# Performance work log

Measured on AMD Instinct MI355X. Metric: run time of the kernel, lower is better.

Reference implementation:

```python
import jax, jax.numpy as jnp
import numpy as np

KERNEL = 3  # 2*half_size + 1 with half_size=1
ITER = 20


def _pool(v):
    # MaxPool2d(kernel=3, stride=1, padding=1) == SAME max reduce_window on NCHW
    return jax.lax.reduce_window(v, -jnp.inf, jax.lax.max,
                                 (1, 1, KERNEL, KERNEL), (1, 1, 1, 1), 'SAME')


def _erode(v):
    return -_pool(-v)


def setup_inputs() -> dict:
    key = jax.random.key(0)
    x = jax.random.normal(key, (16, 1, 1024, 1024), dtype=jnp.float32)
    return {"x": x}


def reference(x):
    skel0 = x - _pool(_erode(x))  # open(x) = dilate(erode(x))

    def step(carry, _):
        xc, skel = carry
        xc = _erode(xc)
        skel = skel + (xc - _pool(_erode(xc)))
        return (xc, skel), None

    (_, skel), _ = jax.lax.scan(step, (x, skel0), None, length=ITER)
    return skel
```

## Files before the change

kernel.cpp:

```cpp
#include <hip/hip_runtime.h>


static constexpr int W = 1024, H = 1024, NIMG = 16;
static constexpr int RCH = 32;
static constexpr int NSTEP = RCH + 16;
static constexpr int WPB = 4;
static constexpr float BIG = 3.0e38f;

__device__ __forceinline__ float min3f(float a, float b, float c) { return fminf(fminf(a, b), c); }
__device__ __forceinline__ float max3f(float a, float b, float c) { return fmaxf(fmaxf(a, b), c); }

__device__ __forceinline__ float dpp_left(float v) {
    return __int_as_float(__builtin_amdgcn_mov_dpp(__float_as_int(v), 0x138, 0xF, 0xF, true));
}
__device__ __forceinline__ float dpp_right(float v) {
    return __int_as_float(__builtin_amdgcn_mov_dpp(__float_as_int(v), 0x130, 0xF, 0xF, true));
}

template<bool FIRST, bool WRITE_E, bool EDGE, bool LE, bool RE>
__device__ __forceinline__
void pipe_step2(int t, int y0, int gx,
                bool leftEdge, bool rightEdge, bool lane_ok,
                const float* __restrict__ in, float* __restrict__ eo,
                float* __restrict__ sk,
                float4 (&OB)[7], float4 (&MB)[7], float4& OD, float4& MD,
                float4 (&acc)[8], float4 (&pf)[2])
{
    float4 cur0, cur1;
    if (!EDGE || (unsigned)t < (unsigned)H)       cur0 = pf[0];
    else                                          cur0 = make_float4(BIG, BIG, BIG, BIG);
    if (!EDGE || (unsigned)(t + 1) < (unsigned)H) cur1 = pf[1];
    else                                          cur1 = make_float4(BIG, BIG, BIG, BIG);
    {
        const int n0 = t + 2, n1 = t + 3;
        if ((!EDGE || (unsigned)n0 < (unsigned)H) && n0 <= y0 + RCH + 7)
            pf[0] = *(const float4*)&in[(size_t)n0 * W + gx];
        if ((!EDGE || (unsigned)n1 < (unsigned)H) && n1 <= y0 + RCH + 7)
            pf[1] = *(const float4*)&in[(size_t)n1 * W + gx];
    }

#pragma unroll
    for (int s = 0; s < 7; ++s) {
        const float4 fOld = OB[s];
        const float4 fMid = MB[s];

        float4 vm0, vm1;
        vm0.x = min3f(fOld.x, fMid.x, cur0.x);
        vm0.y = min3f(fOld.y, fMid.y, cur0.y);
        vm0.z = min3f(fOld.z, fMid.z, cur0.z);
        vm0.w = min3f(fOld.w, fMid.w, cur0.w);
        vm1.x = min3f(fMid.x, cur0.x, cur1.x);
        vm1.y = min3f(fMid.y, cur0.y, cur1.y);
        vm1.z = min3f(fMid.z, cur0.z, cur1.z);
        vm1.w = min3f(fMid.w, cur0.w, cur1.w);
        float l0 = dpp_left(vm0.w), r0 = dpp_right(vm0.x);
        float l1 = dpp_left(vm1.w), r1 = dpp_right(vm1.x);
        if (LE && leftEdge)  { l0 = BIG; l1 = BIG; }
        if (RE && rightEdge) { r0 = BIG; r1 = BIG; }
        float4 en0, en1;
        en0.x = min3f(l0,    vm0.x, vm0.y);
        en0.y = min3f(vm0.x, vm0.y, vm0.z);
        en0.z = min3f(vm0.y, vm0.z, vm0.w);
        en0.w = min3f(vm0.z, vm0.w, r0);
        en1.x = min3f(l1,    vm1.x, vm1.y);
        en1.y = min3f(vm1.x, vm1.y, vm1.z);
        en1.z = min3f(vm1.y, vm1.z, vm1.w);
        en1.w = min3f(vm1.z, vm1.w, r1);

        float4 gOld, gMid;
        if (s < 6) { gOld = OB[s + 1]; gMid = MB[s + 1]; }
        else       { gOld = OD;        gMid = MD;        }
        float4 vx0, vx1;
        if (!EDGE) {
            vx0.x = max3f(gOld.x, gMid.x, en0.x);
            vx0.y = max3f(gOld.y, gMid.y, en0.y);
            vx0.z = max3f(gOld.z, gMid.z, en0.z);
            vx0.w = max3f(gOld.w, gMid.w, en0.w);
            vx1.x = max3f(gMid.x, en0.x, en1.x);
            vx1.y = max3f(gMid.y, en0.y, en1.y);
            vx1.z = max3f(gMid.z, en0.z, en1.z);
            vx1.w = max3f(gMid.w, en0.w, en1.w);
        } else {
            const bool topOK0 = (t - s - 3) >= 0, botOK0 = (t - s - 1) < H;
            const bool topOK1 = (t - s - 2) >= 0, botOK1 = (t - s) < H;
            vx0.x = max3f(topOK0 ? gOld.x : -BIG, gMid.x, botOK0 ? en0.x : -BIG);
            vx0.y = max3f(topOK0 ? gOld.y : -BIG, gMid.y, botOK0 ? en0.y : -BIG);
            vx0.z = max3f(topOK0 ? gOld.z : -BIG, gMid.z, botOK0 ? en0.z : -BIG);
            vx0.w = max3f(topOK0 ? gOld.w : -BIG, gMid.w, botOK0 ? en0.w : -BIG);
            vx1.x = max3f(topOK1 ? gMid.x : -BIG, en0.x, botOK1 ? en1.x : -BIG);
            vx1.y = max3f(topOK1 ? gMid.y : -BIG, en0.y, botOK1 ? en1.y : -BIG);
            vx1.z = max3f(topOK1 ? gMid.z : -BIG, en0.z, botOK1 ? en1.z : -BIG);
            vx1.w = max3f(topOK1 ? gMid.w : -BIG, en0.w, botOK1 ? en1.w : -BIG);
        }
        float dl0 = dpp_left(vx0.w), dr0 = dpp_right(vx0.x);
        float dl1 = dpp_left(vx1.w), dr1 = dpp_right(vx1.x);
        if (LE && leftEdge)  { dl0 = -BIG; dl1 = -BIG; }
        if (RE && rightEdge) { dr0 = -BIG; dr1 = -BIG; }
        float4 dn0, dn1;
        dn0.x = max3f(dl0,   vx0.x, vx0.y);
        dn0.y = max3f(vx0.x, vx0.y, vx0.z);
        dn0.z = max3f(vx0.y, vx0.z, vx0.w);
        dn0.w = max3f(vx0.z, vx0.w, dr0);
        dn1.x = max3f(dl1,   vx1.x, vx1.y);
        dn1.y = max3f(vx1.x, vx1.y, vx1.z);
        dn1.z = max3f(vx1.y, vx1.z, vx1.w);
        dn1.w = max3f(vx1.z, vx1.w, dr1);

        if (FIRST && s == 0) {
            acc[6].x = fOld.x - dn0.x;  acc[6].y = fOld.y - dn0.y;
            acc[6].z = fOld.z - dn0.z;  acc[6].w = fOld.w - dn0.w;
            acc[7].x = fMid.x - dn1.x;  acc[7].y = fMid.y - dn1.y;
            acc[7].z = fMid.z - dn1.z;  acc[7].w = fMid.w - dn1.w;
        } else {
            acc[6 - s].x += fOld.x - dn0.x;  acc[6 - s].y += fOld.y - dn0.y;
            acc[6 - s].z += fOld.z - dn0.z;  acc[6 - s].w += fOld.w - dn0.w;
            acc[7 - s].x += fMid.x - dn1.x;  acc[7 - s].y += fMid.y - dn1.y;
            acc[7 - s].z += fMid.z - dn1.z;  acc[7 - s].w += fMid.w - dn1.w;
        }

        OB[s] = cur0;
        MB[s] = cur1;

        if (s == 6) {
            if (WRITE_E) {
                const int er0 = t - 7, er1 = t - 6;
                if (er0 >= y0 && er0 < y0 + RCH && lane_ok)
                    *(float4*)&eo[(size_t)er0 * W + gx] = en0;
                if (er1 >= y0 && er1 < y0 + RCH && lane_ok)
                    *(float4*)&eo[(size_t)er1 * W + gx] = en1;
            }
            OD = en0;
            MD = en1;
        }
        cur0 = en0;
        cur1 = en1;
    }

    if (t >= y0 + 8) {
        if (lane_ok) {
            *(float4*)&sk[(size_t)(t - 8) * W + gx] = acc[0];
            *(float4*)&sk[(size_t)(t - 7) * W + gx] = acc[1];
        }
    }
#pragma unroll
    for (int j = 0; j < 6; ++j) acc[j] = acc[j + 2];
    if (!FIRST) {
        if (t >= y0 && t < y0 + RCH)
            acc[6] = *(const float4*)&sk[(size_t)t * W + gx];
        if (t + 1 >= y0 && t + 1 < y0 + RCH)
            acc[7] = *(const float4*)&sk[(size_t)(t + 1) * W + gx];
    }
}

template<bool FIRST, bool WRITE_E, bool EDGE, bool LE, bool RE>
__device__ __forceinline__
void sweep(int y0, int gx,
           bool leftEdge, bool rightEdge, bool lane_ok,
           const float* __restrict__ in, float* __restrict__ eo,
           float* __restrict__ sk)
{
    float4 OB[7], MB[7], OD, MD, acc[8], pf[2];
    const float4 big4 = make_float4(BIG, BIG, BIG, BIG);
    const float4 z4   = make_float4(0.f, 0.f, 0.f, 0.f);
#pragma unroll
    for (int s = 0; s < 7; ++s) { OB[s] = big4; MB[s] = big4; }
    OD = big4; MD = big4;
#pragma unroll
    for (int j = 0; j < 8; ++j) acc[j] = z4;
    pf[0] = big4; pf[1] = big4;

    {
        const int r0 = y0 - 8, r1 = y0 - 7;
        if (!EDGE || r0 >= 0) pf[0] = *(const float4*)&in[(size_t)r0 * W + gx];
        if (!EDGE || r1 >= 0) pf[1] = *(const float4*)&in[(size_t)r1 * W + gx];
    }

    const int t0 = y0 - 8;
#pragma unroll 1
    for (int t = t0; t < t0 + NSTEP; t += 2) {
        pipe_step2<FIRST, WRITE_E, EDGE, LE, RE>(t, y0, gx, leftEdge, rightEdge, lane_ok,
                                                 in, eo, sk, OB, MB, OD, MD, acc, pf);
    }
}

template<bool FIRST, bool WRITE_E>
__global__ __launch_bounds__(WPB * 64)
void skel_pipe(const float* __restrict__ ein, float* __restrict__ eout,
               float* __restrict__ skel)
{
    const int lane = threadIdx.x;
    const int bx = blockIdx.x;
    const int y0 = (blockIdx.y * WPB + (int)threadIdx.y) * RCH;
    const int img = blockIdx.z;
    const int x0 = (bx == 4) ? 768 : bx * 240;
    const int gx = x0 + 4 * lane;

    const size_t base = (size_t)img * (size_t)(W * H);
    const float* __restrict__ in = ein + base;
    float* __restrict__ eo = eout + base;
    float* __restrict__ sk = skel + base;

    const bool leftEdge  = (gx == 0);
    const bool rightEdge = (gx + 4 == W);
    const int own_lo = (bx == 0) ? 0 : ((bx == 4) ? 968 : x0 + 8);
    const int own_hi = (bx == 4) ? W : x0 + 248;
    const bool lane_ok = (gx >= own_lo) && (gx < own_hi);

    const bool edge_chunk = !(y0 >= 32 && y0 <= H - RCH - 32);

    if (bx == 0) {
        if (edge_chunk) sweep<FIRST, WRITE_E, true,  true,  false>(y0, gx, leftEdge, rightEdge, lane_ok, in, eo, sk);
        else            sweep<FIRST, WRITE_E, false, true,  false>(y0, gx, leftEdge, rightEdge, lane_ok, in, eo, sk);
    } else if (bx == 4) {
        if (edge_chunk) sweep<FIRST, WRITE_E, true,  false, true >(y0, gx, leftEdge, rightEdge, lane_ok, in, eo, sk);
        else            sweep<FIRST, WRITE_E, false, false, true >(y0, gx, leftEdge, rightEdge, lane_ok, in, eo, sk);
    } else {
        if (edge_chunk) sweep<FIRST, WRITE_E, true,  false, false>(y0, gx, leftEdge, rightEdge, lane_ok, in, eo, sk);
        else            sweep<FIRST, WRITE_E, false, false, false>(y0, gx, leftEdge, rightEdge, lane_ok, in, eo, sk);
    }
}

extern "C" void kernel_launch(void* const* d_in, const int* in_sizes, int n_in,
                              void* d_out, int out_size, void* d_ws, size_t ws_size,
                              hipStream_t stream)
{
    const float* x = (const float*)d_in[0];
    float* skel = (float*)d_out;
    const size_t n = (size_t)NIMG * W * H;

    float* e0 = (float*)d_ws;
    float* e1 = e0 + n;

    dim3 grid(5, H / (RCH * WPB), NIMG);
    dim3 block(64, WPB);

    skel_pipe<true,  true ><<<grid, block, 0, stream>>>(x,  e0, skel);
    skel_pipe<false, true ><<<grid, block, 0, stream>>>(e0, e1, skel);
    skel_pipe<false, false><<<grid, block, 0, stream>>>(e1, e0, skel);
}
```

Baseline: 326.9 us.

## Double row chunk height and split interior sweep into warmup, steady and drain phases

Raises the rows per wave chunk from 32 to 64. This halves the relative cost of the 16-row halo warmup and drain that every chunk recomputes, but also halves the grid size. Interior sweeps now run in phases. A fully unrolled warmup skips the dilate and accumulate work whose results would be discarded. A long steady-state loop then drops the per-row bounds checks on loads and stores, and boundary-checked steps handle the transitions. The risk is lower occupancy and fewer blocks to spread across CUs, plus larger code from the extra template instances.

Result: slower. 359.0 us (+9.8%).

```diff
diff --git a/kernel.cpp b/kernel.cpp
--- a/kernel.cpp
+++ b/kernel.cpp
@@ -2,8 +2,7 @@
 
 
 static constexpr int W = 1024, H = 1024, NIMG = 16;
-static constexpr int RCH = 32;
-static constexpr int NSTEP = RCH + 16;
+static constexpr int RCH = 64;
 static constexpr int WPB = 4;
 static constexpr float BIG = 3.0e38f;
 
@@ -17,7 +16,7 @@
     return __int_as_float(__builtin_amdgcn_mov_dpp(__float_as_int(v), 0x130, 0xF, 0xF, true));
 }
 
-template<bool FIRST, bool WRITE_E, bool EDGE, bool LE, bool RE>
+template<bool FIRST, bool WRITE_E, bool EDGE, bool LE, bool RE, int MODE>
 __device__ __forceinline__
 void pipe_step2(int t, int y0, int gx,
                 bool leftEdge, bool rightEdge, bool lane_ok,
@@ -33,9 +32,9 @@
     else                                          cur1 = make_float4(BIG, BIG, BIG, BIG);
     {
         const int n0 = t + 2, n1 = t + 3;
-        if ((!EDGE || (unsigned)n0 < (unsigned)H) && n0 <= y0 + RCH + 7)
+        if (MODE != 1 || ((!EDGE || (unsigned)n0 < (unsigned)H) && n0 <= y0 + RCH + 7))
             pf[0] = *(const float4*)&in[(size_t)n0 * W + gx];
-        if ((!EDGE || (unsigned)n1 < (unsigned)H) && n1 <= y0 + RCH + 7)
+        if (MODE != 1 || ((!EDGE || (unsigned)n1 < (unsigned)H) && n1 <= y0 + RCH + 7))
             pf[1] = *(const float4*)&in[(size_t)n1 * W + gx];
     }
 
@@ -67,67 +66,76 @@
         en1.z = min3f(vm1.y, vm1.z, vm1.w);
         en1.w = min3f(vm1.z, vm1.w, r1);
 
-        float4 gOld, gMid;
-        if (s < 6) { gOld = OB[s + 1]; gMid = MB[s + 1]; }
-        else       { gOld = OD;        gMid = MD;        }
-        float4 vx0, vx1;
-        if (!EDGE) {
-            vx0.x = max3f(gOld.x, gMid.x, en0.x);
-            vx0.y = max3f(gOld.y, gMid.y, en0.y);
-            vx0.z = max3f(gOld.z, gMid.z, en0.z);
-            vx0.w = max3f(gOld.w, gMid.w, en0.w);
-            vx1.x = max3f(gMid.x, en0.x, en1.x);
-            vx1.y = max3f(gMid.y, en0.y, en1.y);
-            vx1.z = max3f(gMid.z, en0.z, en1.z);
-            vx1.w = max3f(gMid.w, en0.w, en1.w);
-        } else {
-            const bool topOK0 = (t - s - 3) >= 0, botOK0 = (t - s - 1) < H;
-            const bool topOK1 = (t - s - 2) >= 0, botOK1 = (t - s) < H;
-            vx0.x = max3f(topOK0 ? gOld.x : -BIG, gMid.x, botOK0 ? en0.x : -BIG);
-            vx0.y = max3f(topOK0 ? gOld.y : -BIG, gMid.y, botOK0 ? en0.y : -BIG);
-            vx0.z = max3f(topOK0 ? gOld.z : -BIG, gMid.z, botOK0 ? en0.z : -BIG);
-            vx0.w = max3f(topOK0 ? gOld.w : -BIG, gMid.w, botOK0 ? en0.w : -BIG);
-            vx1.x = max3f(topOK1 ? gMid.x : -BIG, en0.x, botOK1 ? en1.x : -BIG);
-            vx1.y = max3f(topOK1 ? gMid.y : -BIG, en0.y, botOK1 ? en1.y : -BIG);
-            vx1.z = max3f(topOK1 ? gMid.z : -BIG, en0.z, botOK1 ? en1.z : -BIG);
-            vx1.w = max3f(topOK1 ? gMid.w : -BIG, en0.w, botOK1 ? en1.w : -BIG);
-        }
-        float dl0 = dpp_left(vx0.w), dr0 = dpp_right(vx0.x);
-        float dl1 = dpp_left(vx1.w), dr1 = dpp_right(vx1.x);
-        if (LE && leftEdge)  { dl0 = -BIG; dl1 = -BIG; }
-        if (RE && rightEdge) { dr0 = -BIG; dr1 = -BIG; }
-        float4 dn0, dn1;
-        dn0.x = max3f(dl0,   vx0.x, vx0.y);
-        dn0.y = max3f(vx0.x, vx0.y, vx0.z);
-        dn0.z = max3f(vx0.y, vx0.z, vx0.w);
-        dn0.w = max3f(vx0.z, vx0.w, dr0);
-        dn1.x = max3f(dl1,   vx1.x, vx1.y);
-        dn1.y = max3f(vx1.x, vx1.y, vx1.z);
-        dn1.z = max3f(vx1.y, vx1.z, vx1.w);
-        dn1.w = max3f(vx1.z, vx1.w, dr1);
-
-        if (FIRST && s == 0) {
-            acc[6].x = fOld.x - dn0.x;  acc[6].y = fOld.y - dn0.y;
-            acc[6].z = fOld.z - dn0.z;  acc[6].w = fOld.w - dn0.w;
-            acc[7].x = fMid.x - dn1.x;  acc[7].y = fMid.y - dn1.y;
-            acc[7].z = fMid.z - dn1.z;  acc[7].w = fMid.w - dn1.w;
-        } else {
-            acc[6 - s].x += fOld.x - dn0.x;  acc[6 - s].y += fOld.y - dn0.y;
-            acc[6 - s].z += fOld.z - dn0.z;  acc[6 - s].w += fOld.w - dn0.w;
-            acc[7 - s].x += fMid.x - dn1.x;  acc[7 - s].y += fMid.y - dn1.y;
-            acc[7 - s].z += fMid.z - dn1.z;  acc[7 - s].w += fMid.w - dn1.w;
+        if (MODE != 0) {
+            float4 gOld, gMid;
+            if (s < 6) { gOld = OB[s + 1]; gMid = MB[s + 1]; }
+            else       { gOld = OD;        gMid = MD;        }
+            float4 vx0, vx1;
+            if (!EDGE) {
+                vx0.x = max3f(gOld.x, gMid.x, en0.x);
+                vx0.y = max3f(gOld.y, gMid.y, en0.y);
+                vx0.z = max3f(gOld.z, gMid.z, en0.z);
+                vx0.w = max3f(gOld.w, gMid.w, en0.w);
+                vx1.x = max3f(gMid.x, en0.x, en1.x);
+                vx1.y = max3f(gMid.y, en0.y, en1.y);
+                vx1.z = max3f(gMid.z, en0.z, en1.z);
+                vx1.w = max3f(gMid.w, en0.w, en1.w);
+            } else {
+                const bool topOK0 = (t - s - 3) >= 0, botOK0 = (t - s - 1) < H;
+                const bool topOK1 = (t - s - 2) >= 0, botOK1 = (t - s) < H;
+                vx0.x = max3f(topOK0 ? gOld.x : -BIG, gMid.x, botOK0 ? en0.x : -BIG);
+                vx0.y = max3f(topOK0 ? gOld.y : -BIG, gMid.y, botOK0 ? en0.y : -BIG);
+                vx0.z = max3f(topOK0 ? gOld.z : -BIG, gMid.z, botOK0 ? en0.z : -BIG);
+                vx0.w = max3f(topOK0 ? gOld.w : -BIG, gMid.w, botOK0 ? en0.w : -BIG);
+                vx1.x = max3f(topOK1 ? gMid.x : -BIG, en0.x, botOK1 ? en1.x : -BIG);
+                vx1.y = max3f(topOK1 ? gMid.y : -BIG, en0.y, botOK1 ? en1.y : -BIG);
+                vx1.z = max3f(topOK1 ? gMid.z : -BIG, en0.z, botOK1 ? en1.z : -BIG);
+                vx1.w = max3f(topOK1 ? gMid.w : -BIG, en0.w, botOK1 ? en1.w : -BIG);
+            }
+            float dl0 = dpp_left(vx0.w), dr0 = dpp_right(vx0.x);
+            float dl1 = dpp_left(vx1.w), dr1 = dpp_right(vx1.x);
+            if (LE && leftEdge)  { dl0 = -BIG; dl1 = -BIG; }
+            if (RE && rightEdge) { dr0 = -BIG; dr1 = -BIG; }
+            float4 dn0, dn1;
+            dn0.x = max3f(dl0,   vx0.x, vx0.y);
+            dn0.y = max3f(vx0.x, vx0.y, vx0.z);
+            dn0.z = max3f(vx0.y, vx0.z, vx0.w);
+            dn0.w = max3f(vx0.z, vx0.w, dr0);
+            dn1.x = max3f(dl1,   vx1.x, vx1.y);
+            dn1.y = max3f(vx1.x, vx1.y, vx1.z);
+            dn1.z = max3f(vx1.y, vx1.z, vx1.w);
+            dn1.w = max3f(vx1.z, vx1.w, dr1);
+
+            if (FIRST && s == 0) {
+                acc[6].x = fOld.x - dn0.x;  acc[6].y = fOld.y - dn0.y;
+                acc[6].z = fOld.z - dn0.z;  acc[6].w = fOld.w - dn0.w;
+                acc[7].x = fMid.x - dn1.x;  acc[7].y = fMid.y - dn1.y;
+                acc[7].z = fMid.z - dn1.z;  acc[7].w = fMid.w - dn1.w;
+            } else {
+                acc[6 - s].x += fOld.x - dn0.x;  acc[6 - s].y += fOld.y - dn0.y;
+                acc[6 - s].z += fOld.z - dn0.z;  acc[6 - s].w += fOld.w - dn0.w;
+                acc[7 - s].x += fMid.x - dn1.x;  acc[7 - s].y += fMid.y - dn1.y;
+                acc[7 - s].z += fMid.z - dn1.z;  acc[7 - s].w += fMid.w - dn1.w;
+            }
         }
 
         OB[s] = cur0;
         MB[s] = cur1;
 
         if (s == 6) {
-            if (WRITE_E) {
+            if (WRITE_E && MODE != 0) {
                 const int er0 = t - 7, er1 = t - 6;
-                if (er0 >= y0 && er0 < y0 + RCH && lane_ok)
-                    *(float4*)&eo[(size_t)er0 * W + gx] = en0;
-                if (er1 >= y0 && er1 < y0 + RCH && lane_ok)
-                    *(float4*)&eo[(size_t)er1 * W + gx] = en1;
+                if (MODE == 2) {
+                    if (lane_ok) {
+                        *(float4*)&eo[(size_t)er0 * W + gx] = en0;
+                        *(float4*)&eo[(size_t)er1 * W + gx] = en1;
+                    }
+                } else {
+                    if (er0 >= y0 && er0 < y0 + RCH && lane_ok)
+                        *(float4*)&eo[(size_t)er0 * W + gx] = en0;
+                    if (er1 >= y0 && er1 < y0 + RCH && lane_ok)
+                        *(float4*)&eo[(size_t)er1 * W + gx] = en1;
+                }
             }
             OD = en0;
             MD = en1;
@@ -136,28 +144,39 @@
         cur1 = en1;
     }
 
-    if (t >= y0 + 8) {
-        if (lane_ok) {
-            *(float4*)&sk[(size_t)(t - 8) * W + gx] = acc[0];
-            *(float4*)&sk[(size_t)(t - 7) * W + gx] = acc[1];
-        }
-    }
-#pragma unroll
-    for (int j = 0; j < 6; ++j) acc[j] = acc[j + 2];
-    if (!FIRST) {
-        if (t >= y0 && t < y0 + RCH)
-            acc[6] = *(const float4*)&sk[(size_t)t * W + gx];
-        if (t + 1 >= y0 && t + 1 < y0 + RCH)
-            acc[7] = *(const float4*)&sk[(size_t)(t + 1) * W + gx];
-    }
-}
-
-template<bool FIRST, bool WRITE_E, bool EDGE, bool LE, bool RE>
+    if (MODE != 0) {
+        if (MODE == 2) {
+            if (lane_ok) {
+                *(float4*)&sk[(size_t)(t - 8) * W + gx] = acc[0];
+                *(float4*)&sk[(size_t)(t - 7) * W + gx] = acc[1];
+            }
+        } else {
+            if (t >= y0 + 8 && lane_ok) {
+                *(float4*)&sk[(size_t)(t - 8) * W + gx] = acc[0];
+                *(float4*)&sk[(size_t)(t - 7) * W + gx] = acc[1];
+            }
+        }
+#pragma unroll
+        for (int j = 0; j < 6; ++j) acc[j] = acc[j + 2];
+        if (!FIRST) {
+            if (MODE == 2) {
+                acc[6] = *(const float4*)&sk[(size_t)t * W + gx];
+                acc[7] = *(const float4*)&sk[(size_t)(t + 1) * W + gx];
+            } else {
+                if (t >= y0 && t < y0 + RCH)
+                    acc[6] = *(const float4*)&sk[(size_t)t * W + gx];
+                if (t + 1 >= y0 && t + 1 < y0 + RCH)
+                    acc[7] = *(const float4*)&sk[(size_t)(t + 1) * W + gx];
+            }
+        }
+    }
+}
+
+template<bool FIRST, bool WRITE_E, bool LE, bool RE>
 __device__ __forceinline__
-void sweep(int y0, int gx,
-           bool leftEdge, bool rightEdge, bool lane_ok,
-           const float* __restrict__ in, float* __restrict__ eo,
-           float* __restrict__ sk)
+void sweep_int(int y0, int gx, bool leftEdge, bool rightEdge, bool lane_ok,
+               const float* __restrict__ in, float* __restrict__ eo,
+               float* __restrict__ sk)
 {
     float4 OB[7], MB[7], OD, MD, acc[8], pf[2];
     const float4 big4 = make_float4(BIG, BIG, BIG, BIG);
@@ -167,20 +186,54 @@
     OD = big4; MD = big4;
 #pragma unroll
     for (int j = 0; j < 8; ++j) acc[j] = z4;
+    pf[0] = *(const float4*)&in[(size_t)(y0 - 8) * W + gx];
+    pf[1] = *(const float4*)&in[(size_t)(y0 - 7) * W + gx];
+
+    int t = y0 - 8;
+#pragma unroll
+    for (int i = 0; i < 4; ++i, t += 2)
+        pipe_step2<FIRST, WRITE_E, false, LE, RE, 0>(t, y0, gx, leftEdge, rightEdge, lane_ok,
+                                                     in, eo, sk, OB, MB, OD, MD, acc, pf);
+#pragma unroll 1
+    for (int i = 0; i < 4; ++i, t += 2)
+        pipe_step2<FIRST, WRITE_E, false, LE, RE, 1>(t, y0, gx, leftEdge, rightEdge, lane_ok,
+                                                     in, eo, sk, OB, MB, OD, MD, acc, pf);
+#pragma unroll 1
+    for (int i = 0; i < 28; ++i, t += 2)
+        pipe_step2<FIRST, WRITE_E, false, LE, RE, 2>(t, y0, gx, leftEdge, rightEdge, lane_ok,
+                                                     in, eo, sk, OB, MB, OD, MD, acc, pf);
+#pragma unroll 1
+    for (int i = 0; i < 4; ++i, t += 2)
+        pipe_step2<FIRST, WRITE_E, false, LE, RE, 1>(t, y0, gx, leftEdge, rightEdge, lane_ok,
+                                                     in, eo, sk, OB, MB, OD, MD, acc, pf);
+}
+
+template<bool FIRST, bool WRITE_E, bool LE, bool RE>
+__device__ __forceinline__
+void sweep_edge(int y0, int gx, bool leftEdge, bool rightEdge, bool lane_ok,
+                const float* __restrict__ in, float* __restrict__ eo,
+                float* __restrict__ sk)
+{
+    float4 OB[7], MB[7], OD, MD, acc[8], pf[2];
+    const float4 big4 = make_float4(BIG, BIG, BIG, BIG);
+    const float4 z4   = make_float4(0.f, 0.f, 0.f, 0.f);
+#pragma unroll
+    for (int s = 0; s < 7; ++s) { OB[s] = big4; MB[s] = big4; }
+    OD = big4; MD = big4;
+#pragma unroll
+    for (int j = 0; j < 8; ++j) acc[j] = z4;
     pf[0] = big4; pf[1] = big4;
-
     {
         const int r0 = y0 - 8, r1 = y0 - 7;
-        if (!EDGE || r0 >= 0) pf[0] = *(const float4*)&in[(size_t)r0 * W + gx];
-        if (!EDGE || r1 >= 0) pf[1] = *(const float4*)&in[(size_t)r1 * W + gx];
-    }
-
-    const int t0 = y0 - 8;
-#pragma unroll 1
-    for (int t = t0; t < t0 + NSTEP; t += 2) {
-        pipe_step2<FIRST, WRITE_E, EDGE, LE, RE>(t, y0, gx, leftEdge, rightEdge, lane_ok,
-                                                 in, eo, sk, OB, MB, OD, MD, acc, pf);
-    }
+        if (r0 >= 0) pf[0] = *(const float4*)&in[(size_t)r0 * W + gx];
+        if (r1 >= 0) pf[1] = *(const float4*)&in[(size_t)r1 * W + gx];
+    }
+
+    int t = y0 - 8;
+#pragma unroll 1
+    for (int i = 0; i < (RCH + 16) / 2; ++i, t += 2)
+        pipe_step2<FIRST, WRITE_E, true, LE, RE, 1>(t, y0, gx, leftEdge, rightEdge, lane_ok,
+                                                    in, eo, sk, OB, MB, OD, MD, acc, pf);
 }
 
 template<bool FIRST, bool WRITE_E>
@@ -206,17 +259,17 @@
     const int own_hi = (bx == 4) ? W : x0 + 248;
     const bool lane_ok = (gx >= own_lo) && (gx < own_hi);
 
-    const bool edge_chunk = !(y0 >= 32 && y0 <= H - RCH - 32);
+    const bool interior = (y0 >= 32 && y0 <= H - RCH - 32);
 
     if (bx == 0) {
-        if (edge_chunk) sweep<FIRST, WRITE_E, true,  true,  false>(y0, gx, leftEdge, rightEdge, lane_ok, in, eo, sk);
-        else            sweep<FIRST, WRITE_E, false, true,  false>(y0, gx, leftEdge, rightEdge, lane_ok, in, eo, sk);
+        if (interior) sweep_int <FIRST, WRITE_E, true,  false>(y0, gx, leftEdge, rightEdge, lane_ok, in, eo, sk);
+        else          sweep_edge<FIRST, WRITE_E, true,  false>(y0, gx, leftEdge, rightEdge, lane_ok, in, eo, sk);
     } else if (bx == 4) {
-        if (edge_chunk) sweep<FIRST, WRITE_E, true,  false, true >(y0, gx, leftEdge, rightEdge, lane_ok, in, eo, sk);
-        else            sweep<FIRST, WRITE_E, false, false, true >(y0, gx, leftEdge, rightEdge, lane_ok, in, eo, sk);
+        if (interior) sweep_int <FIRST, WRITE_E, false, true >(y0, gx, leftEdge, rightEdge, lane_ok, in, eo, sk);
+        else          sweep_edge<FIRST, WRITE_E, false, true >(y0, gx, leftEdge, rightEdge, lane_ok, in, eo, sk);
     } else {
-        if (edge_chunk) sweep<FIRST, WRITE_E, true,  false, false>(y0, gx, leftEdge, rightEdge, lane_ok, in, eo, sk);
-        else            sweep<FIRST, WRITE_E, false, false, false>(y0, gx, leftEdge, rightEdge, lane_ok, in, eo, sk);
+        if (interior) sweep_int <FIRST, WRITE_E, false, false>(y0, gx, leftEdge, rightEdge, lane_ok, in, eo, sk);
+        else          sweep_edge<FIRST, WRITE_E, false, false>(y0, gx, leftEdge, rightEdge, lane_ok, in, eo, sk);
     }
 }
 
```
